# Performance work log

Measured on AMD Instinct MI355X. Metric: run time of the kernel, lower is better.

The kernel has to match this reference:

```python
import jax, jax.numpy as jnp
import numpy as np

N_NODES = 50000
N_EDGES = 600000
N_GRAPHS = 1024
H = 128
VOCAB = 32
NC = 2
BN_EPS = 1e-5


def setup_inputs() -> dict:
    key = jax.random.key(0)
    ks = jax.random.split(key, 16)
    rn = lambda k, s, sc=0.05: jax.random.normal(k, s, jnp.float32) * sc
    inp = {}
    inp["node_feat"] = jax.random.randint(ks[0], (N_NODES,), 0, VOCAB, dtype=jnp.int32)
    inp["edge_src"] = jax.random.randint(ks[1], (N_EDGES,), 0, N_NODES, dtype=jnp.int32)
    inp["edge_dst"] = jax.random.randint(ks[2], (N_EDGES,), 0, N_NODES, dtype=jnp.int32)
    inp["graph_ids"] = jnp.sort(jax.random.randint(ks[3], (N_NODES,), 0, N_GRAPHS, dtype=jnp.int32))
    inp["emb"] = rn(ks[4], (VOCAB, H))
    inp["W1"] = rn(ks[5], (H, H)); inp["b1"] = jnp.zeros((H,), jnp.float32)
    inp["W2"] = rn(ks[6], (H, H)); inp["b2"] = jnp.zeros((H,), jnp.float32)
    inp["e1_w"] = rn(ks[7], (H, H));   inp["e1_b"] = jnp.zeros((H,), jnp.float32)
    inp["e2_w"] = rn(ks[8], (H, H));   inp["e2_b"] = jnp.zeros((H,), jnp.float32)
    inp["e3_w"] = rn(ks[9], (H, 64));  inp["e3_b"] = jnp.zeros((64,), jnp.float32)
    inp["e4_w"] = rn(ks[10], (64, 32)); inp["e4_b"] = jnp.zeros((32,), jnp.float32)
    inp["e5_w"] = rn(ks[11], (32, NC)); inp["e5_b"] = jnp.zeros((NC,), jnp.float32)
    inp["bn0_g"] = jnp.ones((H,), jnp.float32); inp["bn0_b"] = jnp.zeros((H,), jnp.float32)
    inp["bn1_g"] = jnp.ones((H,), jnp.float32); inp["bn1_b"] = jnp.zeros((H,), jnp.float32)
    return inp


def reference(node_feat, edge_src, edge_dst, graph_ids,
              emb, W1, b1, W2, b2,
              e1_w, e1_b, e2_w, e2_b, e3_w, e3_b, e4_w, e4_b, e5_w, e5_b,
              bn0_g, bn0_b, bn1_g, bn1_b):
    ones_e = jnp.ones((N_EDGES,), jnp.float32)
    out_deg = jax.ops.segment_sum(ones_e, edge_src, num_segments=N_NODES)
    in_deg = jax.ops.segment_sum(ones_e, edge_dst, num_segments=N_NODES)
    # DGL GraphConv norm='both': D_out^{-1/2} pre-scale, D_in^{-1/2} post-scale (deg clamped to 1)
    oi = jax.lax.rsqrt(jnp.maximum(out_deg, 1.0))  # [N]
    ii = jax.lax.rsqrt(jnp.maximum(in_deg, 1.0))   # [N]

    def gconv(h, W, b):
        m = (h * oi[:, None])[edge_src]                                   # [E,H] gather
        agg = jax.ops.segment_sum(m, edge_dst, num_segments=N_NODES)      # [N,H] scatter-add
        return (agg * ii[:, None]) @ W + b

    h = emb[node_feat]                       # [N,H] embedding lookup
    h = jax.nn.relu(gconv(h, W1, b1))
    h = jax.nn.relu(gconv(h, W2, b2))

    # dgl.mean_nodes: per-graph mean over nodes
    cnt = jax.ops.segment_sum(jnp.ones((N_NODES,), jnp.float32), graph_ids, num_segments=N_GRAPHS)
    hg = jax.ops.segment_sum(h, graph_ids, num_segments=N_GRAPHS) / jnp.maximum(cnt, 1.0)[:, None]

    def bn(x, g, b):  # BatchNorm1d, training-mode batch stats (biased var)
        mu = x.mean(0)
        var = x.var(0)
        return (x - mu) * jax.lax.rsqrt(var + BN_EPS) * g + b

    def lrelu(x, s):
        return jnp.where(x >= 0, x, s * x)

    h1 = lrelu(bn(hg @ e1_w + e1_b, bn0_g, bn0_b), 0.05)
    h2 = lrelu(bn(h1 @ e2_w + e2_b, bn1_g, bn1_b), 0.05)
    h3 = lrelu(h2 @ e3_w + e3_b, 0.1)
    h4 = lrelu(h3 @ e4_w + e4_b, 0.1)
    y = h4 @ e5_w + e5_b                      # [G, NC]
    return jax.nn.log_softmax(y, axis=1)
```

## Files before the change

### kernel.cpp

```cpp
#include <hip/hip_runtime.h>
#include <hip/hip_bf16.h>
#include <math.h>

#define N_NODES 50000
#define N_PAD   50048
#define N_EDGES 600000
#define N_GRAPHS 1024
#define H 128
#define VOCAB 32
#define BN_EPS 1e-5f
#define SCAN_BLOCKS ((N_NODES + 255) / 256)
#define H1_NODES 64
#define EB ((N_EDGES + 255) / 256)

typedef short bf8_t __attribute__((ext_vector_type(8)));
typedef float f4_t __attribute__((ext_vector_type(4)));

__global__ void k_count_prep(const int* __restrict__ src, int* __restrict__ cntO,
                             const float* __restrict__ emb, const float* __restrict__ W1,
                             float* __restrict__ emb1,
                             const float* __restrict__ W2, __hip_bfloat16* __restrict__ w2t) {
    int b = blockIdx.x;
    int t = threadIdx.x;
    if (b < EB) {
        int i = b * 256 + t;
        if (i < N_EDGES) atomicAdd(&cntO[src[i]], 1);
    } else if (b < EB + 32) {
        if (t < 128) {
            int v = b - EB;
            float acc = 0.f;
            for (int k = 0; k < H; ++k) acc += emb[v * H + k] * W1[k * H + t];
            emb1[v * H + t] = acc;
        }
    } else {
        if (t < 128) {
            int k = b - EB - 32;
            w2t[(size_t)t * H + k] = __float2bfloat16(W2[(size_t)k * H + t]);
        }
    }
}

__global__ void k_hist64(const int* __restrict__ src, const int* __restrict__ dst,
                         const int* __restrict__ feat, const int* __restrict__ cntO,
                         unsigned long long* __restrict__ wc,
                         unsigned char* __restrict__ rank8, int E) {
    int i = blockIdx.x * blockDim.x + threadIdx.x;
    if (i >= E) return;
    int s = src[i], d = dst[i], v = feat[s];
    float o = rsqrtf(fmaxf((float)cntO[s], 1.f));
    unsigned long long q = (unsigned long long)__float2uint_rn(o * 16777216.0f);
    unsigned long long old = atomicAdd(&wc[(size_t)d * VOCAB + v], (1ULL << 40) | q);
    rank8[i] = (unsigned char)(old >> 40);
}

__global__ void k_nodebins(const unsigned long long* __restrict__ wc,
                           int* __restrict__ cntI, unsigned char* __restrict__ binbase,
                           int* __restrict__ bsum, int n) {
    __shared__ int scnt[256];
    int t = threadIdx.x;
    int wave = t >> 6, lane = t & 63;
    int sub = lane >> 5;
    int l32 = lane & 31;
    int nodeBase = blockIdx.x * 256;
#pragma unroll 4
    for (int it = 0; it < 32; ++it) {
        int local = wave * 64 + it * 2 + sub;
        int node = nodeBase + local;
        int c = 0;
        if (node < n && l32 < VOCAB)
            c = (int)(wc[(size_t)node * VOCAB + l32] >> 40);
        int inc = c;
#pragma unroll
        for (int off = 1; off < VOCAB; off <<= 1) {
            int u = __shfl_up(inc, off, 32);
            if (l32 >= off) inc += u;
        }
        if (node < n && l32 < VOCAB)
            binbase[(size_t)node * VOCAB + l32] = (unsigned char)(inc - c);
        if (l32 == VOCAB - 1) scnt[local] = (node < n) ? inc : 0;
    }
    __syncthreads();
    int node = nodeBase + t;
    if (node < n) cntI[node] = scnt[t];
    __shared__ int red[256];
    red[t] = scnt[t];
    __syncthreads();
    for (int off = 128; off > 0; off >>= 1) {
        if (t < off) red[t] += red[t + off];
        __syncthreads();
    }
    if (t == 0) bsum[blockIdx.x] = red[0];
}

__global__ void k_scatterscan(const int* __restrict__ cntI, const int* __restrict__ bsum,
                              int* __restrict__ row_ptr, float* __restrict__ ii,
                              int n, int nb) {
    __shared__ int sb[256];
    __shared__ int sh[256];
    int t = threadIdx.x;
    int bv = (t < nb) ? bsum[t] : 0;
    sb[t] = bv;
    __syncthreads();
    for (int off = 1; off < 256; off <<= 1) {
        int u = (t >= off) ? sb[t - off] : 0;
        __syncthreads();
        sb[t] += u;
        __syncthreads();
    }
    int blockoff = (blockIdx.x == 0) ? 0 : sb[blockIdx.x - 1];
    int i = blockIdx.x * 256 + t;
    int v = (i < n) ? cntI[i] : 0;
    sh[t] = v;
    __syncthreads();
    for (int off = 1; off < 256; off <<= 1) {
        int u = (t >= off) ? sh[t - off] : 0;
        __syncthreads();
        sh[t] += u;
        __syncthreads();
    }
    if (i < n) {
        row_ptr[i] = blockoff + sh[t] - v;
        ii[i] = rsqrtf(fmaxf((float)v, 1.f));
    }
    if (blockIdx.x == 0 && t == 0) row_ptr[n] = sb[nb - 1];
}

#define H1_BLOCKS ((N_NODES + H1_NODES - 1) / H1_NODES)
__global__ void k_fill_h1(const int* __restrict__ src, const int* __restrict__ dst,
                          const int* __restrict__ feat, const int* __restrict__ row_ptr,
                          const unsigned char* __restrict__ binbase,
                          const unsigned char* __restrict__ rank8,
                          int* __restrict__ col,
                          const unsigned long long* __restrict__ wc,
                          const float* __restrict__ emb1,
                          const float* __restrict__ ii, const int* __restrict__ cntO,
                          const float* __restrict__ b1, __hip_bfloat16* __restrict__ h1) {
    __shared__ float wl[H1_NODES * VOCAB];
    __shared__ float sii[H1_NODES], soi[H1_NODES];
    int tid = threadIdx.x;
    if (blockIdx.x < EB) {
        int i = blockIdx.x * 256 + tid;
        if (i < N_EDGES) {
            int s = src[i], d = dst[i], v = feat[s];
            int slot = row_ptr[d] + (int)binbase[(size_t)d * VOCAB + v] + (int)rank8[i];
            col[slot] = s;
        }
        return;
    }
    int hb = blockIdx.x - EB;
    int j = tid & 127;
    int g = tid >> 7;
    float ev[VOCAB];
#pragma unroll
    for (int v = 0; v < VOCAB; ++v) ev[v] = emb1[v * H + j];
    float bj = b1[j];

    int node0 = hb * H1_NODES;
    int nn = min(H1_NODES, N_NODES - node0);
    const unsigned long long* wsrc = wc + (size_t)node0 * VOCAB;
    for (int i = tid; i < nn * VOCAB; i += 256) {
        unsigned long long p = wsrc[i];
        float lo = (float)((unsigned)p & 0xFFFFFFu);
        float hi = (float)((unsigned)(p >> 24) & 0xFFFFu);
        wl[i] = fmaf(lo, 1.0f / 16777216.0f, hi);
    }
    for (int i = tid; i < nn; i += 256) {
        sii[i] = ii[node0 + i];
        soi[i] = rsqrtf(fmaxf((float)cntO[node0 + i], 1.f));
    }
    __syncthreads();

    int rbeg = g * 32;
    int rend = min(rbeg + 32, nn);
    for (int r = rbeg; r < rend; ++r) {
        const float4* wr = (const float4*)(wl + r * VOCAB);
        float acc = 0.f;
#pragma unroll
        for (int q = 0; q < VOCAB / 4; ++q) {
            float4 w4 = wr[q];
            acc += w4.x * ev[4 * q] + w4.y * ev[4 * q + 1]
                 + w4.z * ev[4 * q + 2] + w4.w * ev[4 * q + 3];
        }
        float val = fmaxf(acc * sii[r] + bj, 0.f);
        h1[(size_t)(node0 + r) * H + j] = __float2bfloat16(val * soi[r]);
    }
}

__global__ void k_gather_bf(const __hip_bfloat16* __restrict__ h,
                            const int* __restrict__ row_ptr, const int* __restrict__ col,
                            __hip_bfloat16* __restrict__ out, int n) {
    int gid = blockIdx.x * blockDim.x + threadIdx.x;
    int wid = gid >> 6;
    int lane = gid & 63;
    int node = wid * 4 + (lane >> 4);
    int l16 = lane & 15;
    if (node >= n) return;
    int beg = row_ptr[node];
    int end = row_ptr[node + 1];
    int co = l16 * 8;
    float a0 = 0.f, a1 = 0.f, a2 = 0.f, a3 = 0.f;
    float a4 = 0.f, a5 = 0.f, a6 = 0.f, a7 = 0.f;
    int e = beg;
    for (; e + 8 <= end; e += 8) {
#pragma unroll
        for (int k = 0; k < 8; ++k) {
            int s = col[e + k];
            uint4 v = *(const uint4*)(h + (size_t)s * H + co);
            float2 f0 = __bfloat1622float2(*(__hip_bfloat162*)&v.x);
            float2 f1 = __bfloat1622float2(*(__hip_bfloat162*)&v.y);
            float2 f2 = __bfloat1622float2(*(__hip_bfloat162*)&v.z);
            float2 f3 = __bfloat1622float2(*(__hip_bfloat162*)&v.w);
            a0 += f0.x; a1 += f0.y; a2 += f1.x; a3 += f1.y;
            a4 += f2.x; a5 += f2.y; a6 += f3.x; a7 += f3.y;
        }
    }
    for (; e < end; ++e) {
        int s = col[e];
        uint4 v = *(const uint4*)(h + (size_t)s * H + co);
        float2 f0 = __bfloat1622float2(*(__hip_bfloat162*)&v.x);
        float2 f1 = __bfloat1622float2(*(__hip_bfloat162*)&v.y);
        float2 f2 = __bfloat1622float2(*(__hip_bfloat162*)&v.z);
        float2 f3 = __bfloat1622float2(*(__hip_bfloat162*)&v.w);
        a0 += f0.x; a1 += f0.y; a2 += f1.x; a3 += f1.y;
        a4 += f2.x; a5 += f2.y; a6 += f3.x; a7 += f3.y;
    }
    __hip_bfloat162 o0 = __float22bfloat162_rn(make_float2(a0, a1));
    __hip_bfloat162 o1 = __float22bfloat162_rn(make_float2(a2, a3));
    __hip_bfloat162 o2 = __float22bfloat162_rn(make_float2(a4, a5));
    __hip_bfloat162 o3 = __float22bfloat162_rn(make_float2(a6, a7));
    uint4 ov;
    ov.x = *(unsigned*)&o0; ov.y = *(unsigned*)&o1;
    ov.z = *(unsigned*)&o2; ov.w = *(unsigned*)&o3;
    *(uint4*)(out + (size_t)node * H + co) = ov;
}

__global__ void k_transform_mfma(const __hip_bfloat16* __restrict__ A,
                                 const __hip_bfloat16* __restrict__ WT,
                                 const float* __restrict__ ii,
                                 const float* __restrict__ b,
                                 float* __restrict__ outp, int n) {
    int wave = threadIdx.x >> 6;
    int lane = threadIdx.x & 63;
    int row0 = blockIdx.x * 64 + wave * 16;
    int rl = lane & 15;
    int kg = lane >> 4;
    f4_t acc[8];
#pragma unroll
    for (int t = 0; t < 8; ++t) acc[t] = f4_t{0.f, 0.f, 0.f, 0.f};
    const __hip_bfloat16* arow = A + (size_t)(row0 + rl) * H + kg * 8;
#pragma unroll
    for (int ks = 0; ks < 4; ++ks) {
        bf8_t a = *(const bf8_t*)(arow + ks * 32);
#pragma unroll
        for (int t = 0; t < 8; ++t) {
            bf8_t bf = *(const bf8_t*)(WT + (size_t)(t * 16 + rl) * H + ks * 32 + kg * 8);
            acc[t] = __builtin_amdgcn_mfma_f32_16x16x32_bf16(a, bf, acc[t], 0, 0, 0);
        }
    }
    int rbase = row0 + kg * 4;
#pragma unroll
    for (int r = 0; r < 4; ++r) {
        int node = rbase + r;
        if (node < n) {
            float s = ii[node];
#pragma unroll
            for (int t = 0; t < 8; ++t) {
                int c = t * 16 + rl;
                float v = acc[t][r] * s + b[c];
                outp[(size_t)node * H + c] = fmaxf(v, 0.f);
            }
        }
    }
}

__global__ void k_poolmlp1(const float* __restrict__ h, const int* __restrict__ gid,
                           const float* __restrict__ e1w, const float* __restrict__ e1b,
                           float* __restrict__ t1, int n) {
    __shared__ int bnd[2];
    __shared__ float row[128];
    int g = blockIdx.x, t = threadIdx.x;
    if (t == 0) {
        int lo = 0, hi = n;
        while (lo < hi) { int m = (lo + hi) >> 1; if (gid[m] < g) lo = m + 1; else hi = m; }
        bnd[0] = lo;
        int lo2 = lo, hi2 = n;
        while (lo2 < hi2) { int m = (lo2 + hi2) >> 1; if (gid[m] < g + 1) lo2 = m + 1; else hi2 = m; }
        bnd[1] = lo2;
    }
    __syncthreads();
    int beg = bnd[0], end = bnd[1];
    float s = 0.f;
    for (int i = beg; i < end; ++i) s += h[(size_t)i * H + t];
    row[t] = s / fmaxf((float)(end - beg), 1.f);
    __syncthreads();
    float acc = e1b[t];
    for (int k = 0; k < H; ++k) acc += row[k] * e1w[k * H + t];
    t1[g * H + t] = acc;
}

__global__ void k_bnstat(const float* __restrict__ x, float* __restrict__ stats, int G) {
    int c = blockIdx.x;
    float s = 0.f, s2 = 0.f;
    for (int g = threadIdx.x; g < G; g += blockDim.x) {
        float v = x[g * H + c];
        s += v; s2 += v * v;
    }
    __shared__ float rs[256], rs2[256];
    rs[threadIdx.x] = s; rs2[threadIdx.x] = s2;
    __syncthreads();
    for (int off = 128; off > 0; off >>= 1) {
        if (threadIdx.x < off) { rs[threadIdx.x] += rs[threadIdx.x + off]; rs2[threadIdx.x] += rs2[threadIdx.x + off]; }
        __syncthreads();
    }
    if (threadIdx.x == 0) {
        float mu = rs[0] / G;
        stats[c] = mu;
        stats[H + c] = rs2[0] / G - mu * mu;
    }
}

__global__ void k_mlp2bn(const float* __restrict__ t1, const float* __restrict__ stats,
                         const float* __restrict__ gam, const float* __restrict__ bet,
                         const float* __restrict__ W, const float* __restrict__ bias,
                         float* __restrict__ t2) {
    __shared__ float x[128];
    int g = blockIdx.x, t = threadIdx.x;
    float v = t1[g * H + t];
    v = (v - stats[t]) * rsqrtf(stats[H + t] + BN_EPS) * gam[t] + bet[t];
    x[t] = (v >= 0.f) ? v : 0.05f * v;
    __syncthreads();
    float acc = bias[t];
    for (int k = 0; k < H; ++k) acc += x[k] * W[k * H + t];
    t2[g * H + t] = acc;
}

__global__ void k_head(const float* __restrict__ t2, const float* __restrict__ stats,
                       const float* __restrict__ gam, const float* __restrict__ bet,
                       const float* __restrict__ e3w, const float* __restrict__ e3b,
                       const float* __restrict__ e4w, const float* __restrict__ e4b,
                       const float* __restrict__ e5w, const float* __restrict__ e5b,
                       float* __restrict__ out) {
    __shared__ float x[128], h3[64], h4[32];
    int g = blockIdx.x, t = threadIdx.x;
    float v = t2[g * H + t];
    v = (v - stats[t]) * rsqrtf(stats[H + t] + BN_EPS) * gam[t] + bet[t];
    x[t] = (v >= 0.f) ? v : 0.05f * v;
    __syncthreads();
    if (t < 64) {
        float a = e3b[t];
        for (int k = 0; k < 128; ++k) a += x[k] * e3w[k * 64 + t];
        h3[t] = (a >= 0.f) ? a : 0.1f * a;
    }
    __syncthreads();
    if (t < 32) {
        float a = e4b[t];
        for (int k = 0; k < 64; ++k) a += h3[k] * e4w[k * 32 + t];
        h4[t] = (a >= 0.f) ? a : 0.1f * a;
    }
    __syncthreads();
    if (t == 0) {
        float y0 = e5b[0], y1 = e5b[1];
        for (int k = 0; k < 32; ++k) {
            y0 += h4[k] * e5w[2 * k];
            y1 += h4[k] * e5w[2 * k + 1];
        }
        float m = fmaxf(y0, y1);
        float l = m + logf(expf(y0 - m) + expf(y1 - m));
        out[2 * g] = y0 - l;
        out[2 * g + 1] = y1 - l;
    }
}

extern "C" void kernel_launch(void* const* d_in, const int* in_sizes, int n_in,
                              void* d_out, int out_size, void* d_ws, size_t ws_size,
                              hipStream_t stream) {
    const int*   node_feat = (const int*)d_in[0];
    const int*   edge_src  = (const int*)d_in[1];
    const int*   edge_dst  = (const int*)d_in[2];
    const int*   graph_ids = (const int*)d_in[3];
    const float* emb  = (const float*)d_in[4];
    const float* W1   = (const float*)d_in[5];
    const float* b1   = (const float*)d_in[6];
    const float* W2   = (const float*)d_in[7];
    const float* b2   = (const float*)d_in[8];
    const float* e1_w = (const float*)d_in[9];
    const float* e1_b = (const float*)d_in[10];
    const float* e2_w = (const float*)d_in[11];
    const float* e2_b = (const float*)d_in[12];
    const float* e3_w = (const float*)d_in[13];
    const float* e3_b = (const float*)d_in[14];
    const float* e4_w = (const float*)d_in[15];
    const float* e4_b = (const float*)d_in[16];
    const float* e5_w = (const float*)d_in[17];
    const float* e5_b = (const float*)d_in[18];
    const float* bn0_g = (const float*)d_in[19];
    const float* bn0_b = (const float*)d_in[20];
    const float* bn1_g = (const float*)d_in[21];
    const float* bn1_b = (const float*)d_in[22];
    float* out = (float*)d_out;

    float* ws = (float*)d_ws;
    float* bufA = ws;
    __hip_bfloat16* h1bf = (__hip_bfloat16*)(bufA + (size_t)N_NODES * H);
    __hip_bfloat16* aggbf = h1bf + (size_t)N_NODES * H;
    int*   cntO = (int*)(aggbf + (size_t)N_PAD * H);
    unsigned long long* wc = (unsigned long long*)(cntO + N_NODES);
    float* ii   = (float*)(wc + (size_t)N_NODES * VOCAB);
    int*   cntI = (int*)(ii + N_NODES);
    int*   row_ptr = cntI + N_NODES;
    int*   col  = row_ptr + 50048;
    unsigned char* binbase = (unsigned char*)(col + N_EDGES);
    unsigned char* rank8   = binbase + (size_t)N_NODES * VOCAB;
    float* t1   = (float*)(rank8 + ((N_EDGES + 63) & ~63));
    float* t2   = t1 + N_GRAPHS * H;
    float* stats = t2 + N_GRAPHS * H;
    int*   bsum  = (int*)(stats + 4 * H);
    float* emb1  = (float*)(bsum + 256);
    __hip_bfloat16* w2t = (__hip_bfloat16*)(emb1 + VOCAB * H);

    hipMemsetAsync(cntO, 0, N_NODES * sizeof(int) + (size_t)N_NODES * VOCAB * 8, stream);

    k_count_prep<<<EB + 160, 256, 0, stream>>>(edge_src, cntO, emb, W1, emb1, W2, w2t);
    k_hist64<<<EB, 256, 0, stream>>>(edge_src, edge_dst, node_feat, cntO, wc, rank8, N_EDGES);
    k_nodebins<<<SCAN_BLOCKS, 256, 0, stream>>>(wc, cntI, binbase, bsum, N_NODES);
    k_scatterscan<<<SCAN_BLOCKS, 256, 0, stream>>>(cntI, bsum, row_ptr, ii, N_NODES, SCAN_BLOCKS);
    k_fill_h1<<<EB + H1_BLOCKS, 256, 0, stream>>>(edge_src, edge_dst, node_feat, row_ptr,
                                                  binbase, rank8, col,
                                                  wc, emb1, ii, cntO, b1, h1bf);

    const int gb = (((N_NODES + 3) / 4) * 64 + 255) / 256;
    k_gather_bf<<<gb, 256, 0, stream>>>(h1bf, row_ptr, col, aggbf, N_NODES);
    k_transform_mfma<<<(N_NODES + 63) / 64, 256, 0, stream>>>(aggbf, w2t, ii, b2, bufA, N_NODES);

    k_poolmlp1<<<N_GRAPHS, 128, 0, stream>>>(bufA, graph_ids, e1_w, e1_b, t1, N_NODES);
    k_bnstat<<<H, 256, 0, stream>>>(t1, stats, N_GRAPHS);
    k_mlp2bn<<<N_GRAPHS, 128, 0, stream>>>(t1, stats, bn0_g, bn0_b, e2_w, e2_b, t2);
    k_bnstat<<<H, 256, 0, stream>>>(t2, stats + 2 * H, N_GRAPHS);
    k_head<<<N_GRAPHS, 128, 0, stream>>>(t2, stats + 2 * H, bn1_g, bn1_b,
                                         e3_w, e3_b, e4_w, e4_b, e5_w, e5_b, out);
}
```

Measured before the change: 219.2 us.

## Fuse second-layer neighbor gather with MFMA transform via shared memory tile

Merges the CSR gather kernel and the MFMA weight-transform kernel into one. Each block gathers 64 nodes' aggregated bf16 features into a padded LDS tile, then runs the 16x16x32 bf16 MFMA from LDS. This removes the global write and re-read of the intermediate aggregate buffer and one kernel launch. In exchange, per-node gather parallelism per block is lower and LDS use may reduce occupancy.

```diff
diff --git a/kernel.cpp b/kernel.cpp
--- a/kernel.cpp
+++ b/kernel.cpp
@@ -3,7 +3,6 @@
 #include <math.h>
 
 #define N_NODES 50000
-#define N_PAD   50048
 #define N_EDGES 600000
 #define N_GRAPHS 1024
 #define H 128
@@ -12,6 +11,8 @@
 #define SCAN_BLOCKS ((N_NODES + 255) / 256)
 #define H1_NODES 64
 #define EB ((N_EDGES + 255) / 256)
+#define GM_NODES 64
+#define SROW 136
 
 typedef short bf8_t __attribute__((ext_vector_type(8)));
 typedef float f4_t __attribute__((ext_vector_type(4)));
@@ -186,68 +187,72 @@
     }
 }
 
-__global__ void k_gather_bf(const __hip_bfloat16* __restrict__ h,
-                            const int* __restrict__ row_ptr, const int* __restrict__ col,
-                            __hip_bfloat16* __restrict__ out, int n) {
-    int gid = blockIdx.x * blockDim.x + threadIdx.x;
-    int wid = gid >> 6;
-    int lane = gid & 63;
-    int node = wid * 4 + (lane >> 4);
+__global__ __launch_bounds__(256) void k_gather_mfma(
+        const __hip_bfloat16* __restrict__ h,
+        const int* __restrict__ row_ptr, const int* __restrict__ col,
+        const __hip_bfloat16* __restrict__ WT,
+        const float* __restrict__ ii, const float* __restrict__ b,
+        float* __restrict__ outp, int n) {
+    __shared__ __hip_bfloat16 sA[GM_NODES * SROW];
+    int tid = threadIdx.x;
+    int wave = tid >> 6;
+    int lane = tid & 63;
     int l16 = lane & 15;
-    if (node >= n) return;
-    int beg = row_ptr[node];
-    int end = row_ptr[node + 1];
+    int sub = lane >> 4;
     int co = l16 * 8;
-    float a0 = 0.f, a1 = 0.f, a2 = 0.f, a3 = 0.f;
-    float a4 = 0.f, a5 = 0.f, a6 = 0.f, a7 = 0.f;
-    int e = beg;
-    for (; e + 8 <= end; e += 8) {
-#pragma unroll
-        for (int k = 0; k < 8; ++k) {
-            int s = col[e + k];
-            uint4 v = *(const uint4*)(h + (size_t)s * H + co);
-            float2 f0 = __bfloat1622float2(*(__hip_bfloat162*)&v.x);
-            float2 f1 = __bfloat1622float2(*(__hip_bfloat162*)&v.y);
-            float2 f2 = __bfloat1622float2(*(__hip_bfloat162*)&v.z);
-            float2 f3 = __bfloat1622float2(*(__hip_bfloat162*)&v.w);
-            a0 += f0.x; a1 += f0.y; a2 += f1.x; a3 += f1.y;
-            a4 += f2.x; a5 += f2.y; a6 += f3.x; a7 += f3.y;
-        }
-    }
-    for (; e < end; ++e) {
-        int s = col[e];
-        uint4 v = *(const uint4*)(h + (size_t)s * H + co);
-        float2 f0 = __bfloat1622float2(*(__hip_bfloat162*)&v.x);
-        float2 f1 = __bfloat1622float2(*(__hip_bfloat162*)&v.y);
-        float2 f2 = __bfloat1622float2(*(__hip_bfloat162*)&v.z);
-        float2 f3 = __bfloat1622float2(*(__hip_bfloat162*)&v.w);
-        a0 += f0.x; a1 += f0.y; a2 += f1.x; a3 += f1.y;
-        a4 += f2.x; a5 += f2.y; a6 += f3.x; a7 += f3.y;
-    }
-    __hip_bfloat162 o0 = __float22bfloat162_rn(make_float2(a0, a1));
-    __hip_bfloat162 o1 = __float22bfloat162_rn(make_float2(a2, a3));
-    __hip_bfloat162 o2 = __float22bfloat162_rn(make_float2(a4, a5));
-    __hip_bfloat162 o3 = __float22bfloat162_rn(make_float2(a6, a7));
-    uint4 ov;
-    ov.x = *(unsigned*)&o0; ov.y = *(unsigned*)&o1;
-    ov.z = *(unsigned*)&o2; ov.w = *(unsigned*)&o3;
-    *(uint4*)(out + (size_t)node * H + co) = ov;
-}
-
-__global__ void k_transform_mfma(const __hip_bfloat16* __restrict__ A,
-                                 const __hip_bfloat16* __restrict__ WT,
-                                 const float* __restrict__ ii,
-                                 const float* __restrict__ b,
-                                 float* __restrict__ outp, int n) {
-    int wave = threadIdx.x >> 6;
-    int lane = threadIdx.x & 63;
-    int row0 = blockIdx.x * 64 + wave * 16;
-    int rl = lane & 15;
-    int kg = lane >> 4;
+    int base = blockIdx.x * GM_NODES;
+
+#pragma unroll
+    for (int r = 0; r < 4; ++r) {
+        int local = wave * 16 + r * 4 + sub;
+        int node = base + local;
+        float a0 = 0.f, a1 = 0.f, a2 = 0.f, a3 = 0.f;
+        float a4 = 0.f, a5 = 0.f, a6 = 0.f, a7 = 0.f;
+        if (node < n) {
+            int beg = row_ptr[node];
+            int end = row_ptr[node + 1];
+            int e = beg;
+            for (; e + 8 <= end; e += 8) {
+#pragma unroll
+                for (int k = 0; k < 8; ++k) {
+                    int s = col[e + k];
+                    uint4 v = *(const uint4*)(h + (size_t)s * H + co);
+                    float2 f0 = __bfloat1622float2(*(__hip_bfloat162*)&v.x);
+                    float2 f1 = __bfloat1622float2(*(__hip_bfloat162*)&v.y);
+                    float2 f2 = __bfloat1622float2(*(__hip_bfloat162*)&v.z);
+                    float2 f3 = __bfloat1622float2(*(__hip_bfloat162*)&v.w);
+                    a0 += f0.x; a1 += f0.y; a2 += f1.x; a3 += f1.y;
+                    a4 += f2.x; a5 += f2.y; a6 += f3.x; a7 += f3.y;
+                }
+            }
+            for (; e < end; ++e) {
+                int s = col[e];
+                uint4 v = *(const uint4*)(h + (size_t)s * H + co);
+                float2 f0 = __bfloat1622float2(*(__hip_bfloat162*)&v.x);
+                float2 f1 = __bfloat1622float2(*(__hip_bfloat162*)&v.y);
+                float2 f2 = __bfloat1622float2(*(__hip_bfloat162*)&v.z);
+                float2 f3 = __bfloat1622float2(*(__hip_bfloat162*)&v.w);
+                a0 += f0.x; a1 += f0.y; a2 += f1.x; a3 += f1.y;
+                a4 += f2.x; a5 += f2.y; a6 += f3.x; a7 += f3.y;
+            }
+        }
+        __hip_bfloat162 o0 = __float22bfloat162_rn(make_float2(a0, a1));
+        __hip_bfloat162 o1 = __float22bfloat162_rn(make_float2(a2, a3));
+        __hip_bfloat162 o2 = __float22bfloat162_rn(make_float2(a4, a5));
+        __hip_bfloat162 o3 = __float22bfloat162_rn(make_float2(a6, a7));
+        uint4 ov;
+        ov.x = *(unsigned*)&o0; ov.y = *(unsigned*)&o1;
+        ov.z = *(unsigned*)&o2; ov.w = *(unsigned*)&o3;
+        *(uint4*)(&sA[local * SROW + co]) = ov;
+    }
+    __syncthreads();
+
+    int rl = l16;
+    int kg = sub;
     f4_t acc[8];
 #pragma unroll
     for (int t = 0; t < 8; ++t) acc[t] = f4_t{0.f, 0.f, 0.f, 0.f};
-    const __hip_bfloat16* arow = A + (size_t)(row0 + rl) * H + kg * 8;
+    const __hip_bfloat16* arow = &sA[(wave * 16 + rl) * SROW + kg * 8];
 #pragma unroll
     for (int ks = 0; ks < 4; ++ks) {
         bf8_t a = *(const bf8_t*)(arow + ks * 32);
@@ -257,7 +262,7 @@
             acc[t] = __builtin_amdgcn_mfma_f32_16x16x32_bf16(a, bf, acc[t], 0, 0, 0);
         }
     }
-    int rbase = row0 + kg * 4;
+    int rbase = base + wave * 16 + kg * 4;
 #pragma unroll
     for (int r = 0; r < 4; ++r) {
         int node = rbase + r;
@@ -402,8 +407,7 @@
     float* ws = (float*)d_ws;
     float* bufA = ws;
     __hip_bfloat16* h1bf = (__hip_bfloat16*)(bufA + (size_t)N_NODES * H);
-    __hip_bfloat16* aggbf = h1bf + (size_t)N_NODES * H;
-    int*   cntO = (int*)(aggbf + (size_t)N_PAD * H);
+    int*   cntO = (int*)(h1bf + (size_t)N_NODES * H);
     unsigned long long* wc = (unsigned long long*)(cntO + N_NODES);
     float* ii   = (float*)(wc + (size_t)N_NODES * VOCAB);
     int*   cntI = (int*)(ii + N_NODES);
@@ -428,9 +432,8 @@
                                                   binbase, rank8, col,
                                                   wc, emb1, ii, cntO, b1, h1bf);
 
-    const int gb = (((N_NODES + 3) / 4) * 64 + 255) / 256;
-    k_gather_bf<<<gb, 256, 0, stream>>>(h1bf, row_ptr, col, aggbf, N_NODES);
-    k_transform_mfma<<<(N_NODES + 63) / 64, 256, 0, stream>>>(aggbf, w2t, ii, b2, bufA, N_NODES);
+    k_gather_mfma<<<(N_NODES + GM_NODES - 1) / GM_NODES, 256, 0, stream>>>(
+        h1bf, row_ptr, col, w2t, ii, b2, bufA, N_NODES);
 
     k_poolmlp1<<<N_GRAPHS, 128, 0, stream>>>(bufA, graph_ids, e1_w, e1_b, t1, N_NODES);
     k_bnstat<<<H, 256, 0, stream>>>(t1, stats, N_GRAPHS);
```

Result: no change. 215.2 us (-1.8%).
